# Performance work log

Measured on AMD Instinct MI355X. Metric: run time of the kernel, lower is better.

Reference implementation:

```python
import jax, jax.numpy as jnp
from jax import lax
import numpy as np


def _rnn_tanh_layer(x, W_ih, W_hh, b_ih, b_hh, return_seq):
    # x: [B, T, I]; W_ih: [H, I]; W_hh: [H, H]
    B = x.shape[0]
    H = W_hh.shape[0]
    # Precompute input projection for all timesteps (one big GEMM).
    xw = jnp.einsum('bti,hi->bth', x, W_ih) + b_ih + b_hh  # [B, T, H]
    xw_t = jnp.swapaxes(xw, 0, 1)  # [T, B, H] for scan
    h0 = jnp.zeros((B, H), dtype=x.dtype)

    def step(h, xt):
        h_new = jnp.tanh(xt + h @ W_hh.T)
        return h_new, (h_new if return_seq else None)

    hT, hs = lax.scan(step, h0, xw_t)
    if return_seq:
        return jnp.swapaxes(hs, 0, 1), hT  # [B, T, H], [B, H]
    return None, hT


def setup_inputs() -> dict:
    key = jax.random.key(0)
    ks = jax.random.split(key, 12)
    B, T, I, H1, H2, C = 512, 1024, 32, 128, 64, 10

    def unif(k, shape, fan):
        bound = 1.0 / np.sqrt(fan)
        return jax.random.uniform(k, shape, jnp.float32, -bound, bound)

    return {
        'x': jax.random.normal(ks[0], (B, T, I), jnp.float32),
        'W_ih1': unif(ks[1], (H1, I), H1),
        'W_hh1': unif(ks[2], (H1, H1), H1),
        'b_ih1': unif(ks[3], (H1,), H1),
        'b_hh1': unif(ks[4], (H1,), H1),
        'W_ih2': unif(ks[5], (H2, H1), H2),
        'W_hh2': unif(ks[6], (H2, H2), H2),
        'b_ih2': unif(ks[7], (H2,), H2),
        'b_hh2': unif(ks[8], (H2,), H2),
        'W_fc': unif(ks[9], (C, H2), H2),
        'b_fc': unif(ks[10], (C,), H2),
    }


def reference(x, W_ih1, W_hh1, b_ih1, b_hh1, W_ih2, W_hh2, b_ih2, b_hh2, W_fc, b_fc):
    out1, _h1 = _rnn_tanh_layer(x, W_ih1, W_hh1, b_ih1, b_hh1, return_seq=True)
    _none, h2 = _rnn_tanh_layer(out1, W_ih2, W_hh2, b_ih2, b_hh2, return_seq=False)
    # Dropout(p=0.3) is identity in eval mode.
    logits = h2 @ W_fc.T + b_fc  # [B, 10]
    return logits
```

## Files before the change

### kernel.cpp

```cpp
#include <hip/hip_runtime.h>
#include <stdint.h>


typedef _Float16 f16x8 __attribute__((ext_vector_type(8)));
typedef _Float16 f16x4 __attribute__((ext_vector_type(4)));
typedef float f32x4 __attribute__((ext_vector_type(4)));

#define MFMA_F16(A, B, C) __builtin_amdgcn_mfma_f32_16x16x32_f16((A), (B), (C), 0, 0, 0)

__device__ __forceinline__ float tanh_fast(float x) {
  float t = __builtin_amdgcn_exp2f(x * 2.88539008177792681472f);
  return 1.0f - 2.0f * __builtin_amdgcn_rcpf(t + 1.0f);
}

__device__ __forceinline__ uint32_t pk16(float a, float b) {
  return __builtin_bit_cast(uint32_t, __builtin_amdgcn_cvt_pkrtz(a, b));
}

__device__ __forceinline__ void sync_lds() {
  asm volatile("s_waitcnt lgkmcnt(0)\n\ts_barrier" ::: "memory");
}

__device__ __forceinline__ f16x8 cvt8w(const float* s) {
  f32x4 a = *(const f32x4*)s;
  f32x4 b = *(const f32x4*)(s + 4);
  f16x8 r;
#pragma unroll
  for (int j = 0; j < 4; ++j) { r[j] = (_Float16)a[j]; r[4 + j] = (_Float16)b[j]; }
  return r;
}

__device__ __forceinline__ f16x8 pack_x8(const f32x4& a, const f32x4& b) {
  union { uint32_t u[4]; f16x8 v; } tmp;
  tmp.u[0] = pk16(a[0], a[1]); tmp.u[1] = pk16(a[2], a[3]);
  tmp.u[2] = pk16(b[0], b[1]); tmp.u[3] = pk16(b[2], b[3]);
  return tmp.v;
}

__global__ __launch_bounds__(256) void xw_pre(
    const float* __restrict__ x, const float* __restrict__ Wih1,
    const float* __restrict__ bih1, const float* __restrict__ bhh1,
    uint2* __restrict__ xw)
{
  const int tid  = threadIdx.x;
  const int w    = tid >> 6, lane = tid & 63;
  const int g    = lane >> 4, n = lane & 15;
  const int gb   = blockIdx.x >> 3;
  const int t0   = ((blockIdx.x & 7) << 7) + (w << 5);

  f16x8 aI[8];
  f32x4 bias[8];
#pragma unroll
  for (int m = 0; m < 8; ++m) {
    aI[m] = cvt8w(Wih1 + (m * 16 + n) * 32 + g * 8);
#pragma unroll
    for (int r = 0; r < 4; ++r)
      bias[m][r] = bih1[m * 16 + g * 4 + r] + bhh1[m * 16 + g * 4 + r];
  }

  const float* xp = x + ((size_t)(gb * 16 + n) * 1024 + t0) * 32 + g * 8;
  uint2* xo = xw + (size_t)(gb * 1024 + t0) * 512 + lane;

  f32x4 xa = *(const f32x4*)(xp);
  f32x4 xb = *(const f32x4*)(xp + 4);
  for (int tt = 0; tt < 32; ++tt) {
    f32x4 na, nb;
    if (tt < 31) {
      na = *(const f32x4*)(xp + (tt + 1) * 32);
      nb = *(const f32x4*)(xp + (tt + 1) * 32 + 4);
    }
    f16x8 xf = pack_x8(xa, xb);
#pragma unroll
    for (int m = 0; m < 8; ++m) {
      f32x4 d = MFMA_F16(aI[m], xf, bias[m]);
      xo[tt * 512 + m * 64] = make_uint2(pk16(d[0], d[1]), pk16(d[2], d[3]));
    }
    xa = na; xb = nb;
  }
}

__global__ __attribute__((amdgpu_waves_per_eu(2, 2))) __launch_bounds__(512)
void rnn_rec(
    const float* __restrict__ Whh1,
    const float* __restrict__ Wih2, const float* __restrict__ Whh2,
    const float* __restrict__ bih2, const float* __restrict__ bhh2,
    const float* __restrict__ Wfc,  const float* __restrict__ bfc,
    const uint2* __restrict__ xw,
    float* __restrict__ out)
{
  constexpr int T = 1024, H1 = 128, H2 = 64, BB = 16;
  constexpr int H1_0 = 0,    H1_1 = 4096;
  constexpr int H2_0 = 8192, H2_1 = 10240;
  constexpr int H2F  = 12288;
  __shared__ __align__(16) unsigned char smem[16384];

  const int tid  = threadIdx.x;
  const int w    = tid >> 6;
  const int lane = tid & 63;
  const int g    = lane >> 4;
  const int n    = lane & 15;
  const int b0   = blockIdx.x * BB;

  {
    uint32_t* p = (uint32_t*)smem;
    for (int i = tid; i < 1024; i += 512) p[i] = 0u;
    uint32_t* q = (uint32_t*)(smem + H2_0);
    for (int i = tid; i < 512; i += 512) q[i] = 0u;
  }

  auto tanh_pack = [&](const f32x4& a, uint32_t& lo, uint32_t& hi) {
    lo = pk16(tanh_fast(a[0]), tanh_fast(a[1]));
    hi = pk16(tanh_fast(a[2]), tanh_fast(a[3]));
  };

  __syncthreads();

  const f32x4 zero = {0.f, 0.f, 0.f, 0.f};
  const int lb = lane * 16;

  if (w < 4) {
    f16x8 aU[2][4];
#pragma unroll
    for (int ti = 0; ti < 2; ++ti) {
      const int ch = (2 * w + ti) * 16 + n;
#pragma unroll
      for (int k4 = 0; k4 < 4; ++k4)
        aU[ti][k4] = cvt8w(Whh1 + ch * H1 + k4 * 32 + g * 8);
    }
    int woff[2];
#pragma unroll
    for (int ti = 0; ti < 2; ++ti)
      woff[ti] = w * 1024 + (2 * ti + (g >> 1)) * 256 + n * 16 + (g & 1) * 8;

    const uint2* xwp = xw + (size_t)blockIdx.x * T * 512 + lane;
    const int ti0 = (2 * w) * 64, ti1 = (2 * w + 1) * 64;

    auto cvtC = [](uint2 v) -> f32x4 {
      f16x4 h = __builtin_bit_cast(f16x4, v);
      f32x4 r;
#pragma unroll
      for (int i = 0; i < 4; ++i) r[i] = (float)h[i];
      return r;
    };

    uint2 qA0 = xwp[0 * 512 + ti0], qA1 = xwp[0 * 512 + ti1];
    uint2 qB0 = xwp[1 * 512 + ti0], qB1 = xwp[1 * 512 + ti1];

    auto stepL1 = [&](int t, int cur, uint2& s0, uint2& s1) {
      const char* H1c = (const char*)smem + (cur ? H1_1 : H1_0);
      char*       H1n = (char*)smem + (cur ? H1_0 : H1_1);
      f16x8 b1k0 = *(const f16x8*)(H1c + 0 * 1024 + lb);
      f16x8 b1k1 = *(const f16x8*)(H1c + 1 * 1024 + lb);
      f16x8 b1k2 = *(const f16x8*)(H1c + 2 * 1024 + lb);
      f16x8 b1k3 = *(const f16x8*)(H1c + 3 * 1024 + lb);
      f32x4 accI0 = cvtC(s0), accI1 = cvtC(s1);
      if (t + 2 < T) {
        s0 = xwp[(t + 2) * 512 + ti0];
        s1 = xwp[(t + 2) * 512 + ti1];
      }
      f32x4 aA0 = MFMA_F16(aU[0][0], b1k0, accI0);
      f32x4 aB0 = MFMA_F16(aU[0][2], b1k2, zero);
      f32x4 aA1 = MFMA_F16(aU[1][0], b1k0, accI1);
      f32x4 aB1 = MFMA_F16(aU[1][2], b1k2, zero);
      aA0 = MFMA_F16(aU[0][1], b1k1, aA0);
      aB0 = MFMA_F16(aU[0][3], b1k3, aB0);
      aA1 = MFMA_F16(aU[1][1], b1k1, aA1);
      aB1 = MFMA_F16(aU[1][3], b1k3, aB1);
      {
        f32x4 s0v = aA0 + aB0;
        uint32_t lo, hi;
        tanh_pack(s0v, lo, hi);
        *(uint2*)(H1n + woff[0]) = make_uint2(lo, hi);
      }
      {
        f32x4 s1v = aA1 + aB1;
        uint32_t lo, hi;
        tanh_pack(s1v, lo, hi);
        *(uint2*)(H1n + woff[1]) = make_uint2(lo, hi);
      }
      sync_lds();
    };

    for (int t = 0; t < T; t += 2) {
      stepL1(t + 0, 0, qA0, qA1);
      stepL1(t + 1, 1, qB0, qB1);
    }
  } else {
    const int j = w - 4;
    f16x8 aI2[4], aR2[2];
#pragma unroll
    for (int k4 = 0; k4 < 4; ++k4)
      aI2[k4] = cvt8w(Wih2 + (16 * j + n) * H1 + k4 * 32 + g * 8);
#pragma unroll
    for (int k2 = 0; k2 < 2; ++k2)
      aR2[k2] = cvt8w(Whh2 + (16 * j + n) * H2 + k2 * 32 + g * 8);
    f32x4 bias2;
#pragma unroll
    for (int r = 0; r < 4; ++r)
      bias2[r] = bih2[16 * j + g * 4 + r] + bhh2[16 * j + g * 4 + r];

    const int h2w = (j >> 1) * 1024 + (2 * (j & 1) + (g >> 1)) * 256
                  + n * 16 + (g & 1) * 8;

    auto l2_body = [&](const char* H1c, const char* H2r, f32x4& s) {
      f16x8 b1k0 = *(const f16x8*)(H1c + 0 * 1024 + lb);
      f16x8 b1k1 = *(const f16x8*)(H1c + 1 * 1024 + lb);
      f16x8 b1k2 = *(const f16x8*)(H1c + 2 * 1024 + lb);
      f16x8 b1k3 = *(const f16x8*)(H1c + 3 * 1024 + lb);
      f16x8 b2k0 = *(const f16x8*)(H2r + 0 * 1024 + lb);
      f16x8 b2k1 = *(const f16x8*)(H2r + 1 * 1024 + lb);
      f32x4 cA = MFMA_F16(aI2[0], b1k0, bias2);
      f32x4 cB = MFMA_F16(aI2[1], b1k1, zero);
      f32x4 cC = MFMA_F16(aR2[0], b2k0, zero);
      cA = MFMA_F16(aI2[2], b1k2, cA);
      cB = MFMA_F16(aI2[3], b1k3, cB);
      cC = MFMA_F16(aR2[1], b2k1, cC);
      s = cA + cB + cC;
    };

    auto stepL2 = [&](int t, int cur) {
      if (t > 0) {
        const char* H1c = (const char*)smem + (cur ? H1_1 : H1_0);
        const char* H2r = (const char*)smem + (cur ? H2_0 : H2_1);
        char*       H2w = (char*)smem + (cur ? H2_1 : H2_0);
        f32x4 s;
        l2_body(H1c, H2r, s);
        uint32_t lo, hi;
        tanh_pack(s, lo, hi);
        *(uint2*)(H2w + h2w) = make_uint2(lo, hi);
      }
      sync_lds();
    };

    for (int t = 0; t < T; t += 2) {
      stepL2(t + 0, 0);
      stepL2(t + 1, 1);
    }

    {
      f32x4 s;
      l2_body((const char*)smem + H1_0, (const char*)smem + H2_1, s);
      f32x4 hv;
#pragma unroll
      for (int r = 0; r < 4; ++r) hv[r] = tanh_fast(s[r]);
      *(f32x4*)(smem + H2F + n * 256 + (16 * j + 4 * g) * 4) = hv;
    }
  }

  sync_lds();

  if (tid < BB * 10) {
    const int b = tid / 10, c = tid % 10;
    const float* hrow = (const float*)(smem + H2F + b * 256);
    float acc = bfc[c];
#pragma unroll 8
    for (int k = 0; k < 64; ++k) acc += hrow[k] * Wfc[c * 64 + k];
    out[(size_t)(b0 + b) * 10 + c] = acc;
  }
}

__global__ __launch_bounds__(512) void rnn_fallback(
    const float* __restrict__ x,
    const float* __restrict__ Wih1, const float* __restrict__ Whh1,
    const float* __restrict__ bih1, const float* __restrict__ bhh1,
    const float* __restrict__ Wih2, const float* __restrict__ Whh2,
    const float* __restrict__ bih2, const float* __restrict__ bhh2,
    const float* __restrict__ Wfc,  const float* __restrict__ bfc,
    float* __restrict__ out)
{
  constexpr int T = 1024, I = 32, H1 = 128, H2 = 64, BB = 16;
  constexpr int R1 = 272, R2 = 144;
  constexpr int H1_0 = 0, H1_1 = 4352;
  constexpr int H2_0 = 8704, H2_1 = 11008;
  constexpr int H2F  = 13312;
  __shared__ __align__(16) unsigned char smem[17408];
  const int tid = threadIdx.x, w = tid >> 6, lane = tid & 63;
  const int g = lane >> 4, n = lane & 15, b0 = blockIdx.x * BB;
  {
    uint32_t* p = (uint32_t*)smem;
    for (int i = tid; i < 1088; i += 512) p[i] = 0u;
    uint32_t* q = (uint32_t*)(smem + H2_0);
    for (int i = tid; i < 576; i += 512) q[i] = 0u;
  }
  int roff1[4];
#pragma unroll
  for (int k4 = 0; k4 < 4; ++k4) roff1[k4] = n * R1 + k4 * 64 + g * 16;
  auto tanh_pack = [&](const f32x4& a, uint32_t& lo, uint32_t& hi) {
    lo = pk16(tanh_fast(a[0]), tanh_fast(a[1]));
    hi = pk16(tanh_fast(a[2]), tanh_fast(a[3]));
  };
  __syncthreads();
  const f32x4 zero = {0.f, 0.f, 0.f, 0.f};
  if (w < 4) {
    f16x8 aU[2][4], aI1[2];
    f32x4 bias1[2];
#pragma unroll
    for (int ti = 0; ti < 2; ++ti) {
      const int ch = (2 * w + ti) * 16 + n;
#pragma unroll
      for (int k4 = 0; k4 < 4; ++k4)
        aU[ti][k4] = cvt8w(Whh1 + ch * H1 + k4 * 32 + g * 8);
      aI1[ti] = cvt8w(Wih1 + ch * I + g * 8);
      const int cb = (2 * w + ti) * 16 + g * 4;
#pragma unroll
      for (int r = 0; r < 4; ++r) bias1[ti][r] = bih1[cb + r] + bhh1[cb + r];
    }
    int woff[2];
#pragma unroll
    for (int ti = 0; ti < 2; ++ti)
      woff[ti] = n * R1 + (2 * w + ti) * 32 + g * 8;
    const float* xp = x + (size_t)(b0 + n) * T * I + g * 8;
    f32x4 qa = *(const f32x4*)(xp), qb = *(const f32x4*)(xp + 4);
    f32x4 accI0, accI1;
    {
      f16x8 xf = pack_x8(qa, qb);
      accI0 = MFMA_F16(aI1[0], xf, bias1[0]);
      accI1 = MFMA_F16(aI1[1], xf, bias1[1]);
    }
    for (int t = 0; t < T; ++t) {
      const int cur = t & 1;
      const char* H1c = (const char*)smem + (cur ? H1_1 : H1_0);
      char*       H1n = (char*)smem + (cur ? H1_0 : H1_1);
      f16x8 b1k0 = *(const f16x8*)(H1c + roff1[0]);
      f16x8 b1k1 = *(const f16x8*)(H1c + roff1[1]);
      f16x8 b1k2 = *(const f16x8*)(H1c + roff1[2]);
      f16x8 b1k3 = *(const f16x8*)(H1c + roff1[3]);
      if (t + 1 < T) {
        qa = *(const f32x4*)(xp + (t + 1) * I);
        qb = *(const f32x4*)(xp + (t + 1) * I + 4);
      }
      f32x4 aA0 = MFMA_F16(aU[0][0], b1k0, accI0);
      f32x4 aB0 = MFMA_F16(aU[0][2], b1k2, zero);
      f32x4 aA1 = MFMA_F16(aU[1][0], b1k0, accI1);
      f32x4 aB1 = MFMA_F16(aU[1][2], b1k2, zero);
      aA0 = MFMA_F16(aU[0][1], b1k1, aA0);
      aB0 = MFMA_F16(aU[0][3], b1k3, aB0);
      aA1 = MFMA_F16(aU[1][1], b1k1, aA1);
      aB1 = MFMA_F16(aU[1][3], b1k3, aB1);
      if (t + 1 < T) {
        f16x8 xf = pack_x8(qa, qb);
        accI0 = MFMA_F16(aI1[0], xf, bias1[0]);
        accI1 = MFMA_F16(aI1[1], xf, bias1[1]);
      }
      uint32_t lo, hi;
      f32x4 s0 = aA0 + aB0;
      tanh_pack(s0, lo, hi);
      *(uint2*)(H1n + woff[0]) = make_uint2(lo, hi);
      f32x4 s1 = aA1 + aB1;
      tanh_pack(s1, lo, hi);
      *(uint2*)(H1n + woff[1]) = make_uint2(lo, hi);
      sync_lds();
    }
  } else {
    const int j = w - 4;
    f16x8 aI2[4], aR2[2];
#pragma unroll
    for (int k4 = 0; k4 < 4; ++k4)
      aI2[k4] = cvt8w(Wih2 + (16 * j + n) * H1 + k4 * 32 + g * 8);
#pragma unroll
    for (int k2 = 0; k2 < 2; ++k2)
      aR2[k2] = cvt8w(Whh2 + (16 * j + n) * H2 + k2 * 32 + g * 8);
    f32x4 bias2;
#pragma unroll
    for (int r = 0; r < 4; ++r)
      bias2[r] = bih2[16 * j + g * 4 + r] + bhh2[16 * j + g * 4 + r];
    int roff2[2];
#pragma unroll
    for (int k2 = 0; k2 < 2; ++k2) roff2[k2] = n * R2 + k2 * 64 + g * 16;
    const int woff2 = n * R2 + j * 32 + g * 8;
    auto l2_body = [&](const char* H1c, const char* H2r, f32x4& s) {
      f16x8 b1k0 = *(const f16x8*)(H1c + roff1[0]);
      f16x8 b1k1 = *(const f16x8*)(H1c + roff1[1]);
      f16x8 b1k2 = *(const f16x8*)(H1c + roff1[2]);
      f16x8 b1k3 = *(const f16x8*)(H1c + roff1[3]);
      f16x8 b2k0 = *(const f16x8*)(H2r + roff2[0]);
      f16x8 b2k1 = *(const f16x8*)(H2r + roff2[1]);
      f32x4 cA = MFMA_F16(aI2[0], b1k0, bias2);
      f32x4 cB = MFMA_F16(aI2[1], b1k1, zero);
      f32x4 cC = MFMA_F16(aR2[0], b2k0, zero);
      cA = MFMA_F16(aI2[2], b1k2, cA);
      cB = MFMA_F16(aI2[3], b1k3, cB);
      cC = MFMA_F16(aR2[1], b2k1, cC);
      s = cA + cB + cC;
    };
    for (int t = 0; t < T; ++t) {
      const int cur = t & 1;
      if (t > 0) {
        const char* H1c = (const char*)smem + (cur ? H1_1 : H1_0);
        const char* H2r = (const char*)smem + (cur ? H2_0 : H2_1);
        char*       H2w = (char*)smem + (cur ? H2_1 : H2_0);
        f32x4 s;
        l2_body(H1c, H2r, s);
        uint32_t lo, hi;
        tanh_pack(s, lo, hi);
        *(uint2*)(H2w + woff2) = make_uint2(lo, hi);
      }
      sync_lds();
    }
    {
      f32x4 s;
      l2_body((const char*)smem + H1_0, (const char*)smem + H2_1, s);
      f32x4 hv;
#pragma unroll
      for (int r = 0; r < 4; ++r) hv[r] = tanh_fast(s[r]);
      *(f32x4*)(smem + H2F + n * 256 + (16 * j + 4 * g) * 4) = hv;
    }
  }
  sync_lds();
  if (tid < BB * 10) {
    const int b = tid / 10, c = tid % 10;
    const float* hrow = (const float*)(smem + H2F + b * 256);
    float acc = bfc[c];
#pragma unroll 8
    for (int k = 0; k < 64; ++k) acc += hrow[k] * Wfc[c * 64 + k];
    out[(size_t)(b0 + b) * 10 + c] = acc;
  }
}

extern "C" void kernel_launch(void* const* d_in, const int* in_sizes, int n_in,
                              void* d_out, int out_size, void* d_ws, size_t ws_size,
                              hipStream_t stream) {
  const float* x    = (const float*)d_in[0];
  const float* Wih1 = (const float*)d_in[1];
  const float* Whh1 = (const float*)d_in[2];
  const float* bih1 = (const float*)d_in[3];
  const float* bhh1 = (const float*)d_in[4];
  const float* Wih2 = (const float*)d_in[5];
  const float* Whh2 = (const float*)d_in[6];
  const float* bih2 = (const float*)d_in[7];
  const float* bhh2 = (const float*)d_in[8];
  const float* Wfc  = (const float*)d_in[9];
  const float* bfc  = (const float*)d_in[10];

  const size_t xw_bytes = (size_t)512 * 1024 * 128 * 2;
  if (ws_size >= xw_bytes) {
    uint2* xw = (uint2*)d_ws;
    hipLaunchKernelGGL(xw_pre, dim3(256), dim3(256), 0, stream,
                       x, Wih1, bih1, bhh1, xw);
    hipLaunchKernelGGL(rnn_rec, dim3(512 / 16), dim3(512), 0, stream,
                       Whh1, Wih2, Whh2, bih2, bhh2, Wfc, bfc,
                       (const uint2*)xw, (float*)d_out);
  } else {
    hipLaunchKernelGGL(rnn_fallback, dim3(512 / 16), dim3(512), 0, stream,
                       x, Wih1, Whh1, bih1, bhh1, Wih2, Whh2, bih2, bhh2,
                       Wfc, bfc, (float*)d_out);
  }
}
```

Measured before the change: 426.3 us.

## Prefetch layer-1 outputs one step ahead in layer-2 wavefronts

Layer-2 waves now load the layer-1 hidden state into registers one step early and consume it in the next step. This takes the LDS read of H1 off the critical path of each layer-2 MFMA chain, at the cost of an extra pipeline stage. That stage needs two epilogue steps, two extra barriers in the layer-1 branch to keep barrier counts matched, and a larger zeroed H2 region.

```diff
diff --git a/kernel.cpp b/kernel.cpp
--- a/kernel.cpp
+++ b/kernel.cpp
@@ -105,7 +105,7 @@
     uint32_t* p = (uint32_t*)smem;
     for (int i = tid; i < 1024; i += 512) p[i] = 0u;
     uint32_t* q = (uint32_t*)(smem + H2_0);
-    for (int i = tid; i < 512; i += 512) q[i] = 0u;
+    for (int i = tid; i < 1024; i += 512) q[i] = 0u;
   }
 
   auto tanh_pack = [&](const f32x4& a, uint32_t& lo, uint32_t& hi) {
@@ -185,6 +185,8 @@
       stepL1(t + 0, 0, qA0, qA1);
       stepL1(t + 1, 1, qB0, qB1);
     }
+    sync_lds();
+    sync_lds();
   } else {
     const int j = w - 4;
     f16x8 aI2[4], aR2[2];
@@ -202,32 +204,35 @@
     const int h2w = (j >> 1) * 1024 + (2 * (j & 1) + (g >> 1)) * 256
                   + n * 16 + (g & 1) * 8;
 
-    auto l2_body = [&](const char* H1c, const char* H2r, f32x4& s) {
-      f16x8 b1k0 = *(const f16x8*)(H1c + 0 * 1024 + lb);
-      f16x8 b1k1 = *(const f16x8*)(H1c + 1 * 1024 + lb);
-      f16x8 b1k2 = *(const f16x8*)(H1c + 2 * 1024 + lb);
-      f16x8 b1k3 = *(const f16x8*)(H1c + 3 * 1024 + lb);
-      f16x8 b2k0 = *(const f16x8*)(H2r + 0 * 1024 + lb);
-      f16x8 b2k1 = *(const f16x8*)(H2r + 1 * 1024 + lb);
-      f32x4 cA = MFMA_F16(aI2[0], b1k0, bias2);
-      f32x4 cB = MFMA_F16(aI2[1], b1k1, zero);
-      f32x4 cC = MFMA_F16(aR2[0], b2k0, zero);
-      cA = MFMA_F16(aI2[2], b1k2, cA);
-      cB = MFMA_F16(aI2[3], b1k3, cB);
-      cC = MFMA_F16(aR2[1], b2k1, cC);
-      s = cA + cB + cC;
-    };
+    f16x8 pb0, pb1, pb2, pb3;
 
     auto stepL2 = [&](int t, int cur) {
-      if (t > 0) {
+      f32x4 s;
+      bool live = (t >= 2);
+      if (live) {
+        const char* H2r = (const char*)smem + (cur ? H2_0 : H2_1);
+        f16x8 b2k0 = *(const f16x8*)(H2r + 0 * 1024 + lb);
+        f16x8 b2k1 = *(const f16x8*)(H2r + 1 * 1024 + lb);
+        f32x4 cA = MFMA_F16(aI2[0], pb0, bias2);
+        f32x4 cB = MFMA_F16(aI2[1], pb1, zero);
+        cA = MFMA_F16(aI2[2], pb2, cA);
+        cB = MFMA_F16(aI2[3], pb3, cB);
+        f32x4 cC = MFMA_F16(aR2[0], b2k0, zero);
+        cC = MFMA_F16(aR2[1], b2k1, cC);
+        s = cA + cB + cC;
+      }
+      {
         const char* H1c = (const char*)smem + (cur ? H1_1 : H1_0);
-        const char* H2r = (const char*)smem + (cur ? H2_0 : H2_1);
-        char*       H2w = (char*)smem + (cur ? H2_1 : H2_0);
-        f32x4 s;
-        l2_body(H1c, H2r, s);
+        pb0 = *(const f16x8*)(H1c + 0 * 1024 + lb);
+        pb1 = *(const f16x8*)(H1c + 1 * 1024 + lb);
+        pb2 = *(const f16x8*)(H1c + 2 * 1024 + lb);
+        pb3 = *(const f16x8*)(H1c + 3 * 1024 + lb);
+      }
+      if (live) {
+        char* H2wp = (char*)smem + (cur ? H2_1 : H2_0);
         uint32_t lo, hi;
         tanh_pack(s, lo, hi);
-        *(uint2*)(H2w + h2w) = make_uint2(lo, hi);
+        *(uint2*)(H2wp + h2w) = make_uint2(lo, hi);
       }
       sync_lds();
     };
@@ -236,15 +241,44 @@
       stepL2(t + 0, 0);
       stepL2(t + 1, 1);
     }
-
     {
-      f32x4 s;
-      l2_body((const char*)smem + H1_0, (const char*)smem + H2_1, s);
+      const char* H2r = (const char*)smem + H2_1;
+      f16x8 b2k0 = *(const f16x8*)(H2r + 0 * 1024 + lb);
+      f16x8 b2k1 = *(const f16x8*)(H2r + 1 * 1024 + lb);
+      f32x4 cA = MFMA_F16(aI2[0], pb0, bias2);
+      f32x4 cB = MFMA_F16(aI2[1], pb1, zero);
+      cA = MFMA_F16(aI2[2], pb2, cA);
+      cB = MFMA_F16(aI2[3], pb3, cB);
+      f32x4 cC = MFMA_F16(aR2[0], b2k0, zero);
+      cC = MFMA_F16(aR2[1], b2k1, cC);
+      f32x4 s = cA + cB + cC;
+      const char* H1c = (const char*)smem + H1_0;
+      pb0 = *(const f16x8*)(H1c + 0 * 1024 + lb);
+      pb1 = *(const f16x8*)(H1c + 1 * 1024 + lb);
+      pb2 = *(const f16x8*)(H1c + 2 * 1024 + lb);
+      pb3 = *(const f16x8*)(H1c + 3 * 1024 + lb);
+      uint32_t lo, hi;
+      tanh_pack(s, lo, hi);
+      *(uint2*)((char*)smem + H2_0 + h2w) = make_uint2(lo, hi);
+    }
+    sync_lds();
+    {
+      const char* H2r = (const char*)smem + H2_0;
+      f16x8 b2k0 = *(const f16x8*)(H2r + 0 * 1024 + lb);
+      f16x8 b2k1 = *(const f16x8*)(H2r + 1 * 1024 + lb);
+      f32x4 cA = MFMA_F16(aI2[0], pb0, bias2);
+      f32x4 cB = MFMA_F16(aI2[1], pb1, zero);
+      cA = MFMA_F16(aI2[2], pb2, cA);
+      cB = MFMA_F16(aI2[3], pb3, cB);
+      f32x4 cC = MFMA_F16(aR2[0], b2k0, zero);
+      cC = MFMA_F16(aR2[1], b2k1, cC);
+      f32x4 s = cA + cB + cC;
       f32x4 hv;
 #pragma unroll
       for (int r = 0; r < 4; ++r) hv[r] = tanh_fast(s[r]);
       *(f32x4*)(smem + H2F + n * 256 + (16 * j + 4 * g) * 4) = hv;
     }
+    sync_lds();
   }
 
   sync_lds();
```

New measurement: 432.9 us. About the same (+1.5%).

## Fold tanh exp2 scale into weights and chain MFMA accumulators

Applied to the files above, without the earlier changes.

Pre-multiplies the input and recurrent weights and biases by 2/ln2 so tanh needs no per-element multiply before exp2. It also replaces the split partial-sum MFMA chains with single serial accumulator chains, which removes the vector adds. The serial chain lengthens MFMA dependency latency on the recurrent critical path, and scaling weights before the fp16 conversion slightly changes rounding.

```diff
diff --git a/kernel.cpp b/kernel.cpp
--- a/kernel.cpp
+++ b/kernel.cpp
@@ -8,8 +8,15 @@
 
 #define MFMA_F16(A, B, C) __builtin_amdgcn_mfma_f32_16x16x32_f16((A), (B), (C), 0, 0, 0)
 
+#define TANH_SCALE 2.88539008177792681472f
+
+__device__ __forceinline__ float tanh_s(float s) {
+  float t = __builtin_amdgcn_exp2f(s);
+  return 1.0f - 2.0f * __builtin_amdgcn_rcpf(t + 1.0f);
+}
+
 __device__ __forceinline__ float tanh_fast(float x) {
-  float t = __builtin_amdgcn_exp2f(x * 2.88539008177792681472f);
+  float t = __builtin_amdgcn_exp2f(x * TANH_SCALE);
   return 1.0f - 2.0f * __builtin_amdgcn_rcpf(t + 1.0f);
 }
 
@@ -27,6 +34,18 @@
   f16x8 r;
 #pragma unroll
   for (int j = 0; j < 4; ++j) { r[j] = (_Float16)a[j]; r[4 + j] = (_Float16)b[j]; }
+  return r;
+}
+
+__device__ __forceinline__ f16x8 cvt8ws(const float* s) {
+  f32x4 a = *(const f32x4*)s;
+  f32x4 b = *(const f32x4*)(s + 4);
+  f16x8 r;
+#pragma unroll
+  for (int j = 0; j < 4; ++j) {
+    r[j]     = (_Float16)(a[j] * TANH_SCALE);
+    r[4 + j] = (_Float16)(b[j] * TANH_SCALE);
+  }
   return r;
 }
 
@@ -52,10 +71,10 @@
   f32x4 bias[8];
 #pragma unroll
   for (int m = 0; m < 8; ++m) {
-    aI[m] = cvt8w(Wih1 + (m * 16 + n) * 32 + g * 8);
+    aI[m] = cvt8ws(Wih1 + (m * 16 + n) * 32 + g * 8);
 #pragma unroll
     for (int r = 0; r < 4; ++r)
-      bias[m][r] = bih1[m * 16 + g * 4 + r] + bhh1[m * 16 + g * 4 + r];
+      bias[m][r] = (bih1[m * 16 + g * 4 + r] + bhh1[m * 16 + g * 4 + r]) * TANH_SCALE;
   }
 
   const float* xp = x + ((size_t)(gb * 16 + n) * 1024 + t0) * 32 + g * 8;
@@ -109,13 +128,12 @@
   }
 
   auto tanh_pack = [&](const f32x4& a, uint32_t& lo, uint32_t& hi) {
-    lo = pk16(tanh_fast(a[0]), tanh_fast(a[1]));
-    hi = pk16(tanh_fast(a[2]), tanh_fast(a[3]));
+    lo = pk16(tanh_s(a[0]), tanh_s(a[1]));
+    hi = pk16(tanh_s(a[2]), tanh_s(a[3]));
   };
 
   __syncthreads();
 
-  const f32x4 zero = {0.f, 0.f, 0.f, 0.f};
   const int lb = lane * 16;
 
   if (w < 4) {
@@ -125,7 +143,7 @@
       const int ch = (2 * w + ti) * 16 + n;
 #pragma unroll
       for (int k4 = 0; k4 < 4; ++k4)
-        aU[ti][k4] = cvt8w(Whh1 + ch * H1 + k4 * 32 + g * 8);
+        aU[ti][k4] = cvt8ws(Whh1 + ch * H1 + k4 * 32 + g * 8);
     }
     int woff[2];
 #pragma unroll
@@ -153,29 +171,27 @@
       f16x8 b1k1 = *(const f16x8*)(H1c + 1 * 1024 + lb);
       f16x8 b1k2 = *(const f16x8*)(H1c + 2 * 1024 + lb);
       f16x8 b1k3 = *(const f16x8*)(H1c + 3 * 1024 + lb);
-      f32x4 accI0 = cvtC(s0), accI1 = cvtC(s1);
+      f32x4 acc0 = cvtC(s0), acc1 = cvtC(s1);
       if (t + 2 < T) {
         s0 = xwp[(t + 2) * 512 + ti0];
         s1 = xwp[(t + 2) * 512 + ti1];
       }
-      f32x4 aA0 = MFMA_F16(aU[0][0], b1k0, accI0);
-      f32x4 aB0 = MFMA_F16(aU[0][2], b1k2, zero);
-      f32x4 aA1 = MFMA_F16(aU[1][0], b1k0, accI1);
-      f32x4 aB1 = MFMA_F16(aU[1][2], b1k2, zero);
-      aA0 = MFMA_F16(aU[0][1], b1k1, aA0);
-      aB0 = MFMA_F16(aU[0][3], b1k3, aB0);
-      aA1 = MFMA_F16(aU[1][1], b1k1, aA1);
-      aB1 = MFMA_F16(aU[1][3], b1k3, aB1);
+      acc0 = MFMA_F16(aU[0][0], b1k0, acc0);
+      acc1 = MFMA_F16(aU[1][0], b1k0, acc1);
+      acc0 = MFMA_F16(aU[0][1], b1k1, acc0);
+      acc1 = MFMA_F16(aU[1][1], b1k1, acc1);
+      acc0 = MFMA_F16(aU[0][2], b1k2, acc0);
+      acc1 = MFMA_F16(aU[1][2], b1k2, acc1);
+      acc0 = MFMA_F16(aU[0][3], b1k3, acc0);
+      acc1 = MFMA_F16(aU[1][3], b1k3, acc1);
       {
-        f32x4 s0v = aA0 + aB0;
         uint32_t lo, hi;
-        tanh_pack(s0v, lo, hi);
+        tanh_pack(acc0, lo, hi);
         *(uint2*)(H1n + woff[0]) = make_uint2(lo, hi);
       }
       {
-        f32x4 s1v = aA1 + aB1;
         uint32_t lo, hi;
-        tanh_pack(s1v, lo, hi);
+        tanh_pack(acc1, lo, hi);
         *(uint2*)(H1n + woff[1]) = make_uint2(lo, hi);
       }
       sync_lds();
@@ -190,14 +206,14 @@
     f16x8 aI2[4], aR2[2];
 #pragma unroll
     for (int k4 = 0; k4 < 4; ++k4)
-      aI2[k4] = cvt8w(Wih2 + (16 * j + n) * H1 + k4 * 32 + g * 8);
+      aI2[k4] = cvt8ws(Wih2 + (16 * j + n) * H1 + k4 * 32 + g * 8);
 #pragma unroll
     for (int k2 = 0; k2 < 2; ++k2)
-      aR2[k2] = cvt8w(Whh2 + (16 * j + n) * H2 + k2 * 32 + g * 8);
+      aR2[k2] = cvt8ws(Whh2 + (16 * j + n) * H2 + k2 * 32 + g * 8);
     f32x4 bias2;
 #pragma unroll
     for (int r = 0; r < 4; ++r)
-      bias2[r] = bih2[16 * j + g * 4 + r] + bhh2[16 * j + g * 4 + r];
+      bias2[r] = (bih2[16 * j + g * 4 + r] + bhh2[16 * j + g * 4 + r]) * TANH_SCALE;
 
     const int h2w = (j >> 1) * 1024 + (2 * (j & 1) + (g >> 1)) * 256
                   + n * 16 + (g & 1) * 8;
@@ -209,13 +225,13 @@
       f16x8 b1k3 = *(const f16x8*)(H1c + 3 * 1024 + lb);
       f16x8 b2k0 = *(const f16x8*)(H2r + 0 * 1024 + lb);
       f16x8 b2k1 = *(const f16x8*)(H2r + 1 * 1024 + lb);
-      f32x4 cA = MFMA_F16(aI2[0], b1k0, bias2);
-      f32x4 cB = MFMA_F16(aI2[1], b1k1, zero);
-      f32x4 cC = MFMA_F16(aR2[0], b2k0, zero);
-      cA = MFMA_F16(aI2[2], b1k2, cA);
-      cB = MFMA_F16(aI2[3], b1k3, cB);
-      cC = MFMA_F16(aR2[1], b2k1, cC);
-      s = cA + cB + cC;
+      f32x4 c = MFMA_F16(aI2[0], b1k0, bias2);
+      c = MFMA_F16(aI2[1], b1k1, c);
+      c = MFMA_F16(aI2[2], b1k2, c);
+      c = MFMA_F16(aI2[3], b1k3, c);
+      c = MFMA_F16(aR2[0], b2k0, c);
+      c = MFMA_F16(aR2[1], b2k1, c);
+      s = c;
     };
 
     auto stepL2 = [&](int t, int cur) {
@@ -242,7 +258,7 @@
       l2_body((const char*)smem + H1_0, (const char*)smem + H2_1, s);
       f32x4 hv;
 #pragma unroll
-      for (int r = 0; r < 4; ++r) hv[r] = tanh_fast(s[r]);
+      for (int r = 0; r < 4; ++r) hv[r] = tanh_s(s[r]);
       *(f32x4*)(smem + H2F + n * 256 + (16 * j + 4 * g) * 4) = hv;
     }
   }
```

Result: slower. 479.4 us (+12.4%).
